# Performance work log

Measured on AMD Instinct MI355X. Metric: run time of the kernel, lower is better.

## Reference

```python
import jax, jax.numpy as jnp
import numpy as np

B, S, D = 2, 4096, 2048
H = 16
HD = D // H          # head dim = 128
CHUNK = 64           # chunk size for O(N) chunked linear attention


def setup_inputs() -> dict:
    key = jax.random.key(0)
    ks = jax.random.split(key, 5)
    w = D ** -0.5  # fan-in init scale
    return {
        "x": jax.random.normal(ks[0], (B, S, D), jnp.float32),
        "Wq": jax.random.normal(ks[1], (D, D), jnp.float32) * w,
        "Wk": jax.random.normal(ks[2], (D, D), jnp.float32) * w,
        "Wv": jax.random.normal(ks[3], (D, D), jnp.float32) * w,
        "Wo": jax.random.normal(ks[4], (D, D), jnp.float32) * w,
    }


def _chunk_linear_attn(q, k, v):
    """Causal linear attention (identity feature map), chunked recurrent form.
    q, k, v: [b, h, n, d]. Equivalent to o_t = sum_{s<=t} (q_t . k_s) v_s.
    """
    b, h, n, d = q.shape
    nc = n // CHUNK
    q = q.reshape(b, h, nc, CHUNK, d)
    k = k.reshape(b, h, nc, CHUNK, d)
    v = v.reshape(b, h, nc, CHUNK, d)
    # intra-chunk causal part
    attn = jnp.einsum('bhncd,bhnsd->bhncs', q, k)
    causal = jnp.tril(jnp.ones((CHUNK, CHUNK), dtype=bool))
    attn = jnp.where(causal, attn, jnp.zeros((), attn.dtype))
    o_intra = jnp.einsum('bhncs,bhnsd->bhncd', attn, v)
    # inter-chunk recurrent state: S_i = sum_{j < i} K_j^T V_j  ([d, d] per head)
    kv = jnp.einsum('bhnsd,bhnse->bhnde', k, v)
    S = jnp.cumsum(kv, axis=2) - kv  # exclusive prefix sum over chunks
    o_inter = jnp.einsum('bhncd,bhnde->bhnce', q, S)
    return (o_intra + o_inter).reshape(b, h, n, d)


def reference(x, Wq, Wk, Wv, Wo):
    # bias-free projections (nn.Linear convention: y = x @ W.T)
    q = (x @ Wq.T).reshape(B, S, H, HD).transpose(0, 2, 1, 3)
    k = (x @ Wk.T).reshape(B, S, H, HD).transpose(0, 2, 1, 3)
    v = (x @ Wv.T).reshape(B, S, H, HD).transpose(0, 2, 1, 3)
    scale = HD ** -0.5  # fla chunk_linear_attn default scale on q
    o = _chunk_linear_attn(q * scale, k, v)
    o = o.transpose(0, 2, 1, 3).reshape(B, S, D)
    return o @ Wo.T
```

## Files before the change

### kernel.cpp

```cpp
#include <hip/hip_runtime.h>

typedef unsigned short u16;
typedef __attribute__((ext_vector_type(8))) short short8;
typedef __attribute__((ext_vector_type(8))) unsigned short u16x8;
typedef __attribute__((ext_vector_type(4))) unsigned short u16x4;
typedef __attribute__((ext_vector_type(2))) unsigned short u16x2;
typedef __attribute__((ext_vector_type(4))) float f32x4;

#define NBATCH 2
#define SEQ    4096
#define DIM    2048
#define NHEAD  16
#define HD     128
#define CH     64
#define NC     64
#define MROWS  8192

__device__ __forceinline__ float b2f(u16 u) {
    unsigned x = ((unsigned)u) << 16;
    return __builtin_bit_cast(float, x);
}
__device__ __forceinline__ u16 f2b(float f) {
    unsigned u = __builtin_bit_cast(unsigned, f);
    u += 0x7fffu + ((u >> 16) & 1u);
    return (u16)(u >> 16);
}

__device__ __forceinline__ void gload_lds16(const u16* g, u16* l) {
    __builtin_amdgcn_global_load_lds(
        (const __attribute__((address_space(1))) void*)g,
        (__attribute__((address_space(3))) void*)l, 16, 0, 0);
}

__global__ __launch_bounds__(256) void cast_all(
    const float* __restrict__ x,
    const float* __restrict__ w0, const float* __restrict__ w1,
    const float* __restrict__ w2, const float* __restrict__ w3,
    u16* __restrict__ xo,
    u16* __restrict__ o0, u16* __restrict__ o1,
    u16* __restrict__ o2, u16* __restrict__ o3)
{
    const int blk = blockIdx.x;
    const float* in;
    u16* out;
    long i;
    if (blk < 8192) {
        in = x; out = xo;
        i = (long)blk * 256 + threadIdx.x;
    } else {
        const int seg = (blk - 8192) >> 11;
        in  = seg == 0 ? w0 : seg == 1 ? w1 : seg == 2 ? w2 : w3;
        out = seg == 0 ? o0 : seg == 1 ? o1 : seg == 2 ? o2 : o3;
        i = (long)((blk - 8192) & 2047) * 256 + threadIdx.x;
    }
    f32x4 a = ((const f32x4*)in)[2 * i];
    f32x4 b = ((const f32x4*)in)[2 * i + 1];
    u16x8 o;
#pragma unroll
    for (int j = 0; j < 4; j++) { o[j] = f2b(a[j]); o[4 + j] = f2b(b[j]); }
    ((u16x8*)out)[i] = o;
}

#define GBM 256
#define GBN 256
#define GBK 32
#define BUFE 16384

struct Ctx8 {
    int wave, lane, wr, wc, m16, quad;
    int fl;
    long grA[2];
    int ldso[2];
};

__device__ __forceinline__ Ctx8 ctx8(int K) {
    Ctx8 c;
    const int tid = threadIdx.x;
    c.wave = tid >> 6; c.lane = tid & 63;
    c.wr = c.wave >> 2; c.wc = c.wave & 3;
    c.m16 = c.lane & 15; c.quad = (c.lane >> 4) & 3;
    const int t3 = c.lane >> 3;
    const int u3 = (c.lane & 7) ^ t3;
    const int ml = 2 * t3 + (u3 >> 2);
    const int sl = (u3 & 3) * 8;
#pragma unroll
    for (int i = 0; i < 2; i++) {
        const int bi = 2 * c.wave + i;
        c.grA[i] = (long)(bi * 16 + ml) * K + sl;
        c.ldso[i] = bi * 512 + c.lane * 8;
    }
    const int line = c.m16 >> 1;
    c.fl = line * 64 + ((((c.m16 & 1) << 2) | c.quad) ^ line) * 8;
    return c;
}

template<bool STG, int VMC, bool PRE1>
__device__ __forceinline__ void gstep(
    const Ctx8& c, u16* L, int u,
    short8 (&afC)[4], short8 (&afN)[4],
    short8 (&bfC)[4], short8 (&bfN)[4],
    f32x4 (&acc)[8][4],
    const u16* pA, const u16* pB)
{
    const u16* S0 = L + (u & 3) * BUFE;
    const u16* S1 = L + ((u + 1) & 3) * BUFE;
    u16* SN = L + ((u + 3) & 3) * BUFE;
    const long off = (long)(u + 3) * GBK;

    __builtin_amdgcn_s_barrier();
#pragma unroll
    for (int t = 0; t < 4; t++)
        afN[t] = *(const short8*)&S0[(c.wr * 8 + 4 + t) * 512 + c.fl];
    if (STG) {
        gload_lds16(pA + c.grA[0] + off, SN + c.ldso[0]);
        gload_lds16(pA + c.grA[1] + off, SN + c.ldso[1]);
    }
    __builtin_amdgcn_s_setprio(1);
#pragma unroll
    for (int i = 0; i < 4; i++)
#pragma unroll
        for (int j = 0; j < 4; j++)
            acc[i][j] = __builtin_amdgcn_mfma_f32_16x16x32_bf16(
                afC[i], bfC[j], acc[i][j], 0, 0, 0);
    __builtin_amdgcn_s_setprio(0);

    if (VMC >= 0)
        asm volatile("s_waitcnt vmcnt(%0)" :: "i"(VMC < 0 ? 0 : VMC) : "memory");
    __builtin_amdgcn_s_barrier();
    if (PRE1) {
#pragma unroll
        for (int t = 0; t < 4; t++)
            afC[t] = *(const short8*)&S1[(c.wr * 8 + t) * 512 + c.fl];
#pragma unroll
        for (int t = 0; t < 4; t++)
            bfN[t] = *(const short8*)&S1[8192 + (c.wc * 4 + t) * 512 + c.fl];
    }
    if (STG) {
        gload_lds16(pB + c.grA[0] + off, SN + 8192 + c.ldso[0]);
        gload_lds16(pB + c.grA[1] + off, SN + 8192 + c.ldso[1]);
    }
    __builtin_amdgcn_s_setprio(1);
#pragma unroll
    for (int i = 0; i < 4; i++)
#pragma unroll
        for (int j = 0; j < 4; j++)
            acc[4 + i][j] = __builtin_amdgcn_mfma_f32_16x16x32_bf16(
                afN[i], bfC[j], acc[4 + i][j], 0, 0, 0);
    __builtin_amdgcn_s_setprio(0);
}

__device__ __forceinline__ void kloop8(
    const Ctx8& c, const u16* pA, const u16* pB, int K, u16* L, f32x4 (&acc)[8][4])
{
    const int NT = K >> 5;
#pragma unroll
    for (int t = 0; t < 3; t++) {
        u16* As = L + t * BUFE;
        gload_lds16(pA + c.grA[0] + t * GBK, As + c.ldso[0]);
        gload_lds16(pA + c.grA[1] + t * GBK, As + c.ldso[1]);
        gload_lds16(pB + c.grA[0] + t * GBK, As + 8192 + c.ldso[0]);
        gload_lds16(pB + c.grA[1] + t * GBK, As + 8192 + c.ldso[1]);
    }
    short8 afA[4], afB[4], bfA[4], bfB[4];
    asm volatile("s_waitcnt vmcnt(8)" ::: "memory");
    __builtin_amdgcn_s_barrier();
#pragma unroll
    for (int t = 0; t < 4; t++)
        afA[t] = *(const short8*)&L[(c.wr * 8 + t) * 512 + c.fl];
#pragma unroll
    for (int t = 0; t < 4; t++)
        bfA[t] = *(const short8*)&L[8192 + (c.wc * 4 + t) * 512 + c.fl];

#pragma unroll 1
    for (int u = 0; u < NT - 4; u += 2) {
        gstep<true, 6, true>(c, L, u,     afA, afB, bfA, bfB, acc, pA, pB);
        gstep<true, 6, true>(c, L, u + 1, afA, afB, bfB, bfA, acc, pA, pB);
    }
    gstep<true,  6, true >(c, L, NT - 4, afA, afB, bfA, bfB, acc, pA, pB);
    gstep<false, 4, true >(c, L, NT - 3, afA, afB, bfB, bfA, acc, pA, pB);
    gstep<false, 0, true >(c, L, NT - 2, afA, afB, bfA, bfB, acc, pA, pB);
    gstep<false, -1, false>(c, L, NT - 1, afA, afB, bfB, bfA, acc, pA, pB);
}

__global__ __launch_bounds__(512, 2) void gemm_qkv(
    const u16* __restrict__ A,
    const u16* __restrict__ Wqb, const u16* __restrict__ Wkb, const u16* __restrict__ Wvb,
    u16* __restrict__ q, u16* __restrict__ k, u16* __restrict__ kt,
    u16* __restrict__ vt, float qscale)
{
    __shared__ __align__(16) u16 L[4 * BUFE];
    const Ctx8 c = ctx8(DIM);

    const int w = blockIdx.y >> 3;
    const long row0 = (long)blockIdx.x * GBM;
    const long col0 = (long)(blockIdx.y & 7) * GBN;
    const u16* Bw = w == 0 ? Wqb : w == 1 ? Wkb : Wvb;

    f32x4 acc[8][4];
#pragma unroll
    for (int i = 0; i < 8; i++)
#pragma unroll
        for (int j = 0; j < 4; j++) {
            f32x4 z = {0.f, 0.f, 0.f, 0.f};
            acc[i][j] = z;
        }

    kloop8(c, A + row0 * DIM, Bw + col0 * DIM, DIM, L, acc);

    const float scale = (w == 0) ? qscale : 1.0f;
#pragma unroll
    for (int i = 0; i < 8; i++) {
        const long grow0 = row0 + c.wr * 128 + i * 16 + c.quad * 4;
#pragma unroll
        for (int j = 0; j < 4; j++) {
            const long gcol = col0 + c.wc * 64 + j * 16 + c.m16;
            u16x4 p;
#pragma unroll
            for (int r = 0; r < 4; r++) p[r] = f2b(acc[i][j][r] * scale);
            if (w == 0) {
#pragma unroll
                for (int r = 0; r < 4; r++) q[(grow0 + r) * DIM + gcol] = p[r];
            } else {
                const long b = grow0 >> 12;
                const long t0 = grow0 & (SEQ - 1);
                u16* Ct = (w == 1) ? kt : vt;
                *(u16x4*)(Ct + (b * DIM + gcol) * SEQ + t0) = p;
                if (w == 1) {
#pragma unroll
                    for (int r = 0; r < 4; r++) k[(grow0 + r) * DIM + gcol] = p[r];
                }
            }
        }
    }
}

__global__ __launch_bounds__(512, 2) void gemm_out(
    const u16* __restrict__ A, const u16* __restrict__ Bw, float* __restrict__ C)
{
    __shared__ __align__(16) u16 L[4 * BUFE];
    const Ctx8 c = ctx8(DIM);
    const long row0 = (long)blockIdx.x * GBM;
    const long col0 = (long)blockIdx.y * GBN;

    f32x4 acc[8][4];
#pragma unroll
    for (int i = 0; i < 8; i++)
#pragma unroll
        for (int j = 0; j < 4; j++) {
            f32x4 z = {0.f, 0.f, 0.f, 0.f};
            acc[i][j] = z;
        }

    kloop8(c, A + row0 * DIM, Bw + col0 * DIM, DIM, L, acc);

#pragma unroll
    for (int i = 0; i < 8; i++) {
        const long grow0 = row0 + c.wr * 128 + i * 16 + c.quad * 4;
#pragma unroll
        for (int j = 0; j < 4; j++) {
            const long gcol = col0 + c.wc * 64 + j * 16 + c.m16;
#pragma unroll
            for (int r = 0; r < 4; r++)
                C[(grow0 + r) * DIM + gcol] = acc[i][j][r];
        }
    }
}

__global__ __launch_bounds__(256) void chunk_kv_mfma(
    const u16* __restrict__ Vt, const u16* __restrict__ Kt, u16* __restrict__ KV)
{
    const int tid = threadIdx.x, blk = blockIdx.x;
    const int c = blk & (NC - 1), bh = blk >> 6;
    const int wave = tid >> 6, lane = tid & 63;
    const int wr = wave >> 1, wc = wave & 1;
    const int m16 = lane & 15, quad = lane >> 4;
    const u16* vb = Vt + (long)bh * HD * SEQ + c * CH;
    const u16* kb = Kt + (long)bh * HD * SEQ + c * CH;

    f32x4 acc[4][4];
#pragma unroll
    for (int i = 0; i < 4; i++)
#pragma unroll
        for (int j = 0; j < 4; j++) {
            f32x4 z = {0.f, 0.f, 0.f, 0.f};
            acc[i][j] = z;
        }

#pragma unroll
    for (int tk = 0; tk < 2; tk++) {
        short8 af[4], bf[4];
#pragma unroll
        for (int t = 0; t < 4; t++)
            af[t] = *(const short8*)(vb + (long)(wr * 64 + t * 16 + m16) * SEQ + tk * 32 + quad * 8);
#pragma unroll
        for (int t = 0; t < 4; t++)
            bf[t] = *(const short8*)(kb + (long)(wc * 64 + t * 16 + m16) * SEQ + tk * 32 + quad * 8);
#pragma unroll
        for (int i = 0; i < 4; i++)
#pragma unroll
            for (int j = 0; j < 4; j++)
                acc[i][j] = __builtin_amdgcn_mfma_f32_16x16x32_bf16(
                    af[i], bf[j], acc[i][j], 0, 0, 0);
    }

    u16* outp = KV + (long)blk * (HD * HD);
#pragma unroll
    for (int i = 0; i < 4; i++)
#pragma unroll
        for (int j = 0; j < 4; j++)
#pragma unroll
            for (int r = 0; r < 4; r++)
                outp[(wr * 64 + i * 16 + quad * 4 + r) * HD + wc * 64 + j * 16 + m16]
                    = f2b(acc[i][j][r]);
}

__global__ __launch_bounds__(256) void kv_prefix(u16* __restrict__ KV)
{
    const int bh  = blockIdx.x >> 4;
    const int sub = blockIdx.x & 15;
    const long base = (long)bh * NC * (HD * HD) + (sub * 256 + threadIdx.x) * 4;
    float s0 = 0.f, s1 = 0.f, s2 = 0.f, s3 = 0.f;
#pragma unroll 4
    for (int c = 0; c < NC; c++) {
        u16* p = KV + base + (long)c * (HD * HD);
        u16x4 v = *(u16x4*)p;
        u16x4 w;
        w[0] = f2b(s0); w[1] = f2b(s1); w[2] = f2b(s2); w[3] = f2b(s3);
        *(u16x4*)p = w;
        s0 += b2f(v[0]); s1 += b2f(v[1]); s2 += b2f(v[2]); s3 += b2f(v[3]);
    }
}

#define AMP 72

__global__ __launch_bounds__(256) void chunk_out_mfma(
    const u16* __restrict__ Q, const u16* __restrict__ Kn,
    const u16* __restrict__ Vt, const u16* __restrict__ Sb, u16* __restrict__ O)
{
    __shared__ __align__(16) u16 Am[CH * AMP];

    const int tid = threadIdx.x, blk = blockIdx.x;
    const int c = blk & (NC - 1), bh = blk >> 6;
    const int h = bh & (NHEAD - 1), b = bh >> 4;
    const long rowbase = (long)b * SEQ + (long)c * CH;
    const int wave = tid >> 6, lane = tid & 63;
    const int m16 = lane & 15, quad = lane >> 4;

    const u16* qrow = Q  + (rowbase + wave * 16 + m16) * DIM + h * HD;
    const u16* krow = Kn + rowbase * DIM + h * HD;

    short8 qa[4];
#pragma unroll
    for (int dk = 0; dk < 4; dk++)
        qa[dk] = *(const short8*)(qrow + dk * 32 + quad * 8);

    f32x4 acc1[4];
#pragma unroll
    for (int jt = 0; jt < 4; jt++) {
        f32x4 z = {0.f, 0.f, 0.f, 0.f};
        acc1[jt] = z;
    }
#pragma unroll
    for (int dk = 0; dk < 4; dk++)
#pragma unroll
        for (int jt = 0; jt < 4; jt++) {
            short8 bb = *(const short8*)(krow + (long)(jt * 16 + m16) * DIM + dk * 32 + quad * 8);
            acc1[jt] = __builtin_amdgcn_mfma_f32_16x16x32_bf16(qa[dk], bb, acc1[jt], 0, 0, 0);
        }
    const int mbase = wave * 16 + quad * 4;
#pragma unroll
    for (int jt = 0; jt < 4; jt++) {
        const int j = jt * 16 + m16;
#pragma unroll
        for (int r = 0; r < 4; r++) {
            float v = (j <= mbase + r) ? acc1[jt][r] : 0.f;
            Am[(mbase + r) * AMP + j] = f2b(v);
        }
    }

    f32x4 acc[8];
#pragma unroll
    for (int et = 0; et < 8; et++) {
        f32x4 z = {0.f, 0.f, 0.f, 0.f};
        acc[et] = z;
    }
    const u16* Sg = Sb + (long)blk * (HD * HD);
#pragma unroll
    for (int dk = 0; dk < 4; dk++)
#pragma unroll
        for (int et = 0; et < 8; et++) {
            short8 sb = *(const short8*)(Sg + (et * 16 + m16) * HD + dk * 32 + quad * 8);
            acc[et] = __builtin_amdgcn_mfma_f32_16x16x32_bf16(qa[dk], sb, acc[et], 0, 0, 0);
        }

    __syncthreads();
    const u16* vb = Vt + (long)bh * HD * SEQ + c * CH;
#pragma unroll
    for (int tk = 0; tk < 2; tk++) {
        short8 a = *(const short8*)&Am[(wave * 16 + m16) * AMP + tk * 32 + quad * 8];
#pragma unroll
        for (int et = 0; et < 8; et++) {
            short8 vbf = *(const short8*)(vb + (long)(et * 16 + m16) * SEQ + tk * 32 + quad * 8);
            acc[et] = __builtin_amdgcn_mfma_f32_16x16x32_bf16(a, vbf, acc[et], 0, 0, 0);
        }
    }

#pragma unroll
    for (int et = 0; et < 8; et++) {
        const int e = et * 16 + m16;
#pragma unroll
        for (int r = 0; r < 4; r++) {
            const int m = wave * 16 + quad * 4 + r;
            O[(rowbase + m) * DIM + h * HD + e] = f2b(acc[et][r]);
        }
    }
}

extern "C" void kernel_launch(void* const* d_in, const int* in_sizes, int n_in,
                              void* d_out, int out_size, void* d_ws, size_t ws_size,
                              hipStream_t stream)
{
    (void)in_sizes; (void)n_in; (void)out_size; (void)ws_size;
    const float* x  = (const float*)d_in[0];
    const float* Wq = (const float*)d_in[1];
    const float* Wk = (const float*)d_in[2];
    const float* Wv = (const float*)d_in[3];
    const float* Wo = (const float*)d_in[4];
    float* out = (float*)d_out;

    const long NE = (long)MROWS * DIM;
    const long WE = (long)DIM * DIM;
    u16* xb  = (u16*)d_ws;
    u16* Wqb = xb  + NE;
    u16* Wkb = Wqb + WE;
    u16* Wvb = Wkb + WE;
    u16* Wob = Wvb + WE;
    u16* q   = Wob + WE;
    u16* k   = q + NE;
    u16* vt  = k + NE;
    u16* kv  = vt + NE;
    u16* o   = xb;
    u16* kt  = (u16*)d_out;

    hipLaunchKernelGGL(cast_all, dim3(16384), dim3(256), 0, stream,
                       x, Wq, Wk, Wv, Wo, xb, Wqb, Wkb, Wvb, Wob);

    const float qscale = 0.08838834764831845f;

    hipLaunchKernelGGL(gemm_qkv, dim3(MROWS / GBM, 24), dim3(512), 0, stream,
                       xb, Wqb, Wkb, Wvb, q, k, kt, vt, qscale);

    hipLaunchKernelGGL(chunk_kv_mfma, dim3(NBATCH * NHEAD * NC), dim3(256), 0, stream, vt, kt, kv);
    hipLaunchKernelGGL(kv_prefix,     dim3(512),                 dim3(256), 0, stream, kv);
    hipLaunchKernelGGL(chunk_out_mfma,dim3(NBATCH * NHEAD * NC), dim3(256), 0, stream, q, k, vt, kv, o);

    hipLaunchKernelGGL(gemm_out, dim3(MROWS / GBM, DIM / GBN), dim3(512), 0, stream, o, Wob, out);
}
```

Baseline: 532.6 us.

## Restructure QKV GEMM k-loop to one barrier per step with full A-fragment prefetch

Replaces the two-half gstep with gstep2, which takes a single barrier per K-step. It loads that step's B fragments, prefetches all eight A fragments for the next stage, and issues all four global-to-LDS loads for stage u+3 together. The 32 MFMAs then run in one block. This halves the barrier count and simplifies the vmcnt accounting, with the aim of cutting synchronisation stalls. In exchange, the B fragments are read right before use, so their latency has less to hide behind, and the larger A double buffer raises register pressure.

```diff
diff --git a/kernel.cpp b/kernel.cpp
--- a/kernel.cpp
+++ b/kernel.cpp
@@ -94,58 +94,41 @@
     return c;
 }
 
-template<bool STG, int VMC, bool PRE1>
-__device__ __forceinline__ void gstep(
+template<bool STG, int VMC, bool PREA>
+__device__ __forceinline__ void gstep2(
     const Ctx8& c, u16* L, int u,
-    short8 (&afC)[4], short8 (&afN)[4],
-    short8 (&bfC)[4], short8 (&bfN)[4],
-    f32x4 (&acc)[8][4],
-    const u16* pA, const u16* pB)
-{
-    const u16* S0 = L + (u & 3) * BUFE;
-    const u16* S1 = L + ((u + 1) & 3) * BUFE;
-    u16* SN = L + ((u + 3) & 3) * BUFE;
-    const long off = (long)(u + 3) * GBK;
-
-    __builtin_amdgcn_s_barrier();
-#pragma unroll
-    for (int t = 0; t < 4; t++)
-        afN[t] = *(const short8*)&S0[(c.wr * 8 + 4 + t) * 512 + c.fl];
-    if (STG) {
-        gload_lds16(pA + c.grA[0] + off, SN + c.ldso[0]);
-        gload_lds16(pA + c.grA[1] + off, SN + c.ldso[1]);
-    }
-    __builtin_amdgcn_s_setprio(1);
-#pragma unroll
-    for (int i = 0; i < 4; i++)
-#pragma unroll
-        for (int j = 0; j < 4; j++)
-            acc[i][j] = __builtin_amdgcn_mfma_f32_16x16x32_bf16(
-                afC[i], bfC[j], acc[i][j], 0, 0, 0);
-    __builtin_amdgcn_s_setprio(0);
-
+    short8 (&aC)[8], short8 (&aN)[8], short8 (&b)[4],
+    f32x4 (&acc)[8][4], const u16* pA, const u16* pB)
+{
     if (VMC >= 0)
         asm volatile("s_waitcnt vmcnt(%0)" :: "i"(VMC < 0 ? 0 : VMC) : "memory");
     __builtin_amdgcn_s_barrier();
-    if (PRE1) {
-#pragma unroll
-        for (int t = 0; t < 4; t++)
-            afC[t] = *(const short8*)&S1[(c.wr * 8 + t) * 512 + c.fl];
-#pragma unroll
-        for (int t = 0; t < 4; t++)
-            bfN[t] = *(const short8*)&S1[8192 + (c.wc * 4 + t) * 512 + c.fl];
+    asm volatile("" ::: "memory");
+    const u16* SC = L + (u & 3) * BUFE;
+#pragma unroll
+    for (int t = 0; t < 4; t++)
+        b[t] = *(const short8*)&SC[8192 + (c.wc * 4 + t) * 512 + c.fl];
+    if (PREA) {
+        const u16* SN = L + ((u + 1) & 3) * BUFE;
+#pragma unroll
+        for (int t = 0; t < 8; t++)
+            aN[t] = *(const short8*)&SN[(c.wr * 8 + t) * 512 + c.fl];
     }
     if (STG) {
-        gload_lds16(pB + c.grA[0] + off, SN + 8192 + c.ldso[0]);
-        gload_lds16(pB + c.grA[1] + off, SN + 8192 + c.ldso[1]);
+        u16* SD = L + ((u + 3) & 3) * BUFE;
+        const long off = (long)(u + 3) * GBK;
+        gload_lds16(pA + c.grA[0] + off, SD + c.ldso[0]);
+        gload_lds16(pA + c.grA[1] + off, SD + c.ldso[1]);
+        gload_lds16(pB + c.grA[0] + off, SD + 8192 + c.ldso[0]);
+        gload_lds16(pB + c.grA[1] + off, SD + 8192 + c.ldso[1]);
     }
     __builtin_amdgcn_s_setprio(1);
 #pragma unroll
-    for (int i = 0; i < 4; i++)
-#pragma unroll
-        for (int j = 0; j < 4; j++)
-            acc[4 + i][j] = __builtin_amdgcn_mfma_f32_16x16x32_bf16(
-                afN[i], bfC[j], acc[4 + i][j], 0, 0, 0);
+    for (int j = 0; j < 4; j++)
+#pragma unroll
+        for (int i = 0; i < 8; i++)
+            acc[i][j] = __builtin_amdgcn_mfma_f32_16x16x32_bf16(
+                aC[i], b[j], acc[i][j], 0, 0, 0);
     __builtin_amdgcn_s_setprio(0);
 }
 
@@ -161,25 +144,23 @@
         gload_lds16(pB + c.grA[0] + t * GBK, As + 8192 + c.ldso[0]);
         gload_lds16(pB + c.grA[1] + t * GBK, As + 8192 + c.ldso[1]);
     }
-    short8 afA[4], afB[4], bfA[4], bfB[4];
+    short8 aP[8], aQ[8], b[4];
     asm volatile("s_waitcnt vmcnt(8)" ::: "memory");
     __builtin_amdgcn_s_barrier();
-#pragma unroll
-    for (int t = 0; t < 4; t++)
-        afA[t] = *(const short8*)&L[(c.wr * 8 + t) * 512 + c.fl];
-#pragma unroll
-    for (int t = 0; t < 4; t++)
-        bfA[t] = *(const short8*)&L[8192 + (c.wc * 4 + t) * 512 + c.fl];
+    asm volatile("" ::: "memory");
+#pragma unroll
+    for (int t = 0; t < 8; t++)
+        aP[t] = *(const short8*)&L[(c.wr * 8 + t) * 512 + c.fl];
 
 #pragma unroll 1
     for (int u = 0; u < NT - 4; u += 2) {
-        gstep<true, 6, true>(c, L, u,     afA, afB, bfA, bfB, acc, pA, pB);
-        gstep<true, 6, true>(c, L, u + 1, afA, afB, bfB, bfA, acc, pA, pB);
-    }
-    gstep<true,  6, true >(c, L, NT - 4, afA, afB, bfA, bfB, acc, pA, pB);
-    gstep<false, 4, true >(c, L, NT - 3, afA, afB, bfB, bfA, acc, pA, pB);
-    gstep<false, 0, true >(c, L, NT - 2, afA, afB, bfA, bfB, acc, pA, pB);
-    gstep<false, -1, false>(c, L, NT - 1, afA, afB, bfB, bfA, acc, pA, pB);
+        gstep2<true, 4, true>(c, L, u,     aP, aQ, b, acc, pA, pB);
+        gstep2<true, 4, true>(c, L, u + 1, aQ, aP, b, acc, pA, pB);
+    }
+    gstep2<true,  4, true >(c, L, NT - 4, aP, aQ, b, acc, pA, pB);
+    gstep2<false, 4, true >(c, L, NT - 3, aQ, aP, b, acc, pA, pB);
+    gstep2<false, 0, true >(c, L, NT - 2, aP, aQ, b, acc, pA, pB);
+    gstep2<false, -1, false>(c, L, NT - 1, aQ, aP, b, acc, pA, pB);
 }
 
 __global__ __launch_bounds__(512, 2) void gemm_qkv(
```

Measured after the change: 543.3 us. 1.02x slower.

## Use 128x128 tiles with 4-wave blocks for the QKV projection GEMM

Applied to the files above, without the earlier changes.

Replaces the 256x256-tile, 8-wave QKV GEMM with a new 128x128-tile, 4-wave kernel that has its own 4-slot LDS pipeline and swizzled loads. The grid grows from 32x24 to 64x48 blocks, which is meant to fill the GPU's CUs better and cut tail effects. In exchange, each block reuses loaded data less, so global and L2 traffic per FLOP goes up, and the wait counts of the pipeline change.

```diff
diff --git a/kernel.cpp b/kernel.cpp
--- a/kernel.cpp
+++ b/kernel.cpp
@@ -61,6 +61,161 @@
     ((u16x8*)out)[i] = o;
 }
 
+#define QBM 128
+#define QBN 128
+#define QBK 32
+#define QSLOT 8192
+
+struct Ctx4 {
+    int wave, lane, wr, wc, m16, quad;
+    int fl;
+    long gr[2];
+    int ldso[2];
+};
+
+__device__ __forceinline__ Ctx4 ctx4(int K) {
+    Ctx4 c;
+    const int tid = threadIdx.x;
+    c.wave = tid >> 6; c.lane = tid & 63;
+    c.wr = c.wave >> 1; c.wc = c.wave & 1;
+    c.m16 = c.lane & 15; c.quad = c.lane >> 4;
+    const int key = (c.m16 >> 1) & 3;
+    c.fl = c.m16 * 32 + ((c.quad ^ key) * 8);
+#pragma unroll
+    for (int i = 0; i < 2; i++) {
+        const int idx = tid + 256 * i;
+        const int row = idx >> 2;
+        const int ps  = idx & 3;
+        c.gr[i]   = (long)row * K + ((ps ^ ((row >> 1) & 3)) * 8);
+        c.ldso[i] = idx * 8;
+    }
+    return c;
+}
+
+template<bool STG, int VMC, bool PRE>
+__device__ __forceinline__ void kstep4(
+    const Ctx4& c, u16* L, int u,
+    short8 (&aC)[4], short8 (&bC)[4],
+    short8 (&aN)[4], short8 (&bN)[4],
+    f32x4 (&acc)[4][4], const u16* pA, const u16* pB)
+{
+    if (VMC >= 0)
+        asm volatile("s_waitcnt vmcnt(%0)" :: "i"(VMC < 0 ? 0 : VMC) : "memory");
+    __builtin_amdgcn_s_barrier();
+    asm volatile("" ::: "memory");
+    if (PRE) {
+        const u16* SN = L + ((u + 1) & 3) * QSLOT;
+#pragma unroll
+        for (int t = 0; t < 4; t++)
+            aN[t] = *(const short8*)&SN[c.wr * 2048 + t * 512 + c.fl];
+#pragma unroll
+        for (int t = 0; t < 4; t++)
+            bN[t] = *(const short8*)&SN[4096 + c.wc * 2048 + t * 512 + c.fl];
+    }
+    if (STG) {
+        u16* SD = L + ((u + 3) & 3) * QSLOT;
+        const long off = (long)(u + 3) * QBK;
+        gload_lds16(pA + c.gr[0] + off, SD + c.ldso[0]);
+        gload_lds16(pA + c.gr[1] + off, SD + c.ldso[1]);
+        gload_lds16(pB + c.gr[0] + off, SD + 4096 + c.ldso[0]);
+        gload_lds16(pB + c.gr[1] + off, SD + 4096 + c.ldso[1]);
+    }
+    __builtin_amdgcn_s_setprio(1);
+#pragma unroll
+    for (int i = 0; i < 4; i++)
+#pragma unroll
+        for (int j = 0; j < 4; j++)
+            acc[i][j] = __builtin_amdgcn_mfma_f32_16x16x32_bf16(
+                aC[i], bC[j], acc[i][j], 0, 0, 0);
+    __builtin_amdgcn_s_setprio(0);
+}
+
+__device__ __forceinline__ void kloop4(
+    const Ctx4& c, const u16* pA, const u16* pB, int K, u16* L, f32x4 (&acc)[4][4])
+{
+    const int NT = K >> 5;
+#pragma unroll
+    for (int t = 0; t < 3; t++) {
+        u16* SD = L + t * QSLOT;
+        gload_lds16(pA + c.gr[0] + t * QBK, SD + c.ldso[0]);
+        gload_lds16(pA + c.gr[1] + t * QBK, SD + c.ldso[1]);
+        gload_lds16(pB + c.gr[0] + t * QBK, SD + 4096 + c.ldso[0]);
+        gload_lds16(pB + c.gr[1] + t * QBK, SD + 4096 + c.ldso[1]);
+    }
+    short8 aP[4], bP[4], aQ[4], bQ[4];
+    asm volatile("s_waitcnt vmcnt(8)" ::: "memory");
+    __builtin_amdgcn_s_barrier();
+    asm volatile("" ::: "memory");
+#pragma unroll
+    for (int t = 0; t < 4; t++)
+        aP[t] = *(const short8*)&L[c.wr * 2048 + t * 512 + c.fl];
+#pragma unroll
+    for (int t = 0; t < 4; t++)
+        bP[t] = *(const short8*)&L[4096 + c.wc * 2048 + t * 512 + c.fl];
+
+#pragma unroll 1
+    for (int u = 0; u < NT - 4; u += 2) {
+        kstep4<true, 4, true>(c, L, u,     aP, bP, aQ, bQ, acc, pA, pB);
+        kstep4<true, 4, true>(c, L, u + 1, aQ, bQ, aP, bP, acc, pA, pB);
+    }
+    kstep4<true,  4, true >(c, L, NT - 4, aP, bP, aQ, bQ, acc, pA, pB);
+    kstep4<false, 4, true >(c, L, NT - 3, aQ, bQ, aP, bP, acc, pA, pB);
+    kstep4<false, 0, true >(c, L, NT - 2, aP, bP, aQ, bQ, acc, pA, pB);
+    kstep4<false, -1, false>(c, L, NT - 1, aQ, bQ, aP, bP, acc, pA, pB);
+}
+
+__global__ __launch_bounds__(256, 2) void gemm_qkv(
+    const u16* __restrict__ A,
+    const u16* __restrict__ Wqb, const u16* __restrict__ Wkb, const u16* __restrict__ Wvb,
+    u16* __restrict__ q, u16* __restrict__ k, u16* __restrict__ kt,
+    u16* __restrict__ vt, float qscale)
+{
+    __shared__ __align__(16) u16 L[4 * QSLOT];
+    const Ctx4 c = ctx4(DIM);
+
+    const int w = blockIdx.y >> 4;
+    const long row0 = (long)blockIdx.x * QBM;
+    const long col0 = (long)(blockIdx.y & 15) * QBN;
+    const u16* Bw = w == 0 ? Wqb : w == 1 ? Wkb : Wvb;
+
+    f32x4 acc[4][4];
+#pragma unroll
+    for (int i = 0; i < 4; i++)
+#pragma unroll
+        for (int j = 0; j < 4; j++) {
+            f32x4 z = {0.f, 0.f, 0.f, 0.f};
+            acc[i][j] = z;
+        }
+
+    kloop4(c, A + row0 * DIM, Bw + col0 * DIM, DIM, L, acc);
+
+    const float scale = (w == 0) ? qscale : 1.0f;
+#pragma unroll
+    for (int i = 0; i < 4; i++) {
+        const long grow0 = row0 + c.wr * 64 + i * 16 + c.quad * 4;
+#pragma unroll
+        for (int j = 0; j < 4; j++) {
+            const long gcol = col0 + c.wc * 64 + j * 16 + c.m16;
+            u16x4 p;
+#pragma unroll
+            for (int r = 0; r < 4; r++) p[r] = f2b(acc[i][j][r] * scale);
+            if (w == 0) {
+#pragma unroll
+                for (int r = 0; r < 4; r++) q[(grow0 + r) * DIM + gcol] = p[r];
+            } else {
+                const long b = grow0 >> 12;
+                const long t0 = grow0 & (SEQ - 1);
+                u16* Ct = (w == 1) ? kt : vt;
+                *(u16x4*)(Ct + (b * DIM + gcol) * SEQ + t0) = p;
+                if (w == 1) {
+#pragma unroll
+                    for (int r = 0; r < 4; r++) k[(grow0 + r) * DIM + gcol] = p[r];
+                }
+            }
+        }
+    }
+}
+
 #define GBM 256
 #define GBN 256
 #define GBK 32
@@ -180,58 +335,6 @@
     gstep<false, 4, true >(c, L, NT - 3, afA, afB, bfB, bfA, acc, pA, pB);
     gstep<false, 0, true >(c, L, NT - 2, afA, afB, bfA, bfB, acc, pA, pB);
     gstep<false, -1, false>(c, L, NT - 1, afA, afB, bfB, bfA, acc, pA, pB);
-}
-
-__global__ __launch_bounds__(512, 2) void gemm_qkv(
-    const u16* __restrict__ A,
-    const u16* __restrict__ Wqb, const u16* __restrict__ Wkb, const u16* __restrict__ Wvb,
-    u16* __restrict__ q, u16* __restrict__ k, u16* __restrict__ kt,
-    u16* __restrict__ vt, float qscale)
-{
-    __shared__ __align__(16) u16 L[4 * BUFE];
-    const Ctx8 c = ctx8(DIM);
-
-    const int w = blockIdx.y >> 3;
-    const long row0 = (long)blockIdx.x * GBM;
-    const long col0 = (long)(blockIdx.y & 7) * GBN;
-    const u16* Bw = w == 0 ? Wqb : w == 1 ? Wkb : Wvb;
-
-    f32x4 acc[8][4];
-#pragma unroll
-    for (int i = 0; i < 8; i++)
-#pragma unroll
-        for (int j = 0; j < 4; j++) {
-            f32x4 z = {0.f, 0.f, 0.f, 0.f};
-            acc[i][j] = z;
-        }
-
-    kloop8(c, A + row0 * DIM, Bw + col0 * DIM, DIM, L, acc);
-
-    const float scale = (w == 0) ? qscale : 1.0f;
-#pragma unroll
-    for (int i = 0; i < 8; i++) {
-        const long grow0 = row0 + c.wr * 128 + i * 16 + c.quad * 4;
-#pragma unroll
-        for (int j = 0; j < 4; j++) {
-            const long gcol = col0 + c.wc * 64 + j * 16 + c.m16;
-            u16x4 p;
-#pragma unroll
-            for (int r = 0; r < 4; r++) p[r] = f2b(acc[i][j][r] * scale);
-            if (w == 0) {
-#pragma unroll
-                for (int r = 0; r < 4; r++) q[(grow0 + r) * DIM + gcol] = p[r];
-            } else {
-                const long b = grow0 >> 12;
-                const long t0 = grow0 & (SEQ - 1);
-                u16* Ct = (w == 1) ? kt : vt;
-                *(u16x4*)(Ct + (b * DIM + gcol) * SEQ + t0) = p;
-                if (w == 1) {
-#pragma unroll
-                    for (int r = 0; r < 4; r++) k[(grow0 + r) * DIM + gcol] = p[r];
-                }
-            }
-        }
-    }
 }
 
 __global__ __launch_bounds__(512, 2) void gemm_out(
@@ -447,7 +550,7 @@
 
     const float qscale = 0.08838834764831845f;
 
-    hipLaunchKernelGGL(gemm_qkv, dim3(MROWS / GBM, 24), dim3(512), 0, stream,
+    hipLaunchKernelGGL(gemm_qkv, dim3(MROWS / QBM, 48), dim3(256), 0, stream,
                        xb, Wqb, Wkb, Wvb, q, k, kt, vt, qscale);
 
     hipLaunchKernelGGL(chunk_kv_mfma, dim3(NBATCH * NHEAD * NC), dim3(256), 0, stream, vt, kt, kv);
```

New measurement: 592.2 us. 1.11x slower.
